# Performance work log

Measured on AMD Instinct MI355X. Metric: run time of the kernel, lower is better.

Reference implementation:

```python
import jax, jax.numpy as jnp
import numpy as np

BATCH, SEQ, D_MODEL = 2, 4096, 1024
D_STATE, EXPAND = 64, 2
D_INNER = D_MODEL * EXPAND


def setup_inputs() -> dict:
    key = jax.random.key(0)
    ks = jax.random.split(key, 12)
    s = 0.02
    return {
        "x": jax.random.normal(ks[0], (BATCH, SEQ, D_MODEL), dtype=jnp.float32),
        "W_in": jax.random.normal(ks[1], (D_MODEL, 2 * D_INNER), dtype=jnp.float32) * s,
        "b_in": jnp.zeros((2 * D_INNER,), dtype=jnp.float32),
        "W_xp": jax.random.normal(ks[2], (D_INNER, D_STATE), dtype=jnp.float32) * s,
        "b_xp": jnp.zeros((D_STATE,), dtype=jnp.float32),
        "W_dt": jax.random.normal(ks[3], (D_INNER, D_MODEL), dtype=jnp.float32) * s,
        "b_dt": jnp.zeros((D_MODEL,), dtype=jnp.float32),
        "W_out": jax.random.normal(ks[4], (D_INNER, D_MODEL), dtype=jnp.float32) * s,
        "b_out": jnp.zeros((D_MODEL,), dtype=jnp.float32),
        "A_log": jax.random.normal(ks[5], (D_STATE,), dtype=jnp.float32),
        "D": jax.random.normal(ks[6], (D_MODEL,), dtype=jnp.float32),
    }


def _silu(v):
    return v * jax.nn.sigmoid(v)


def reference(x, W_in, b_in, W_xp, b_xp, W_dt, b_dt, W_out, b_out, A_log, D):
    # in_proj -> split into inner stream and residual gate
    xr = x @ W_in + b_in                       # [B,S,2*d_inner]
    x_inner, res = jnp.split(xr, 2, axis=-1)   # each [B,S,d_inner]
    x_inner = _silu(x_inner)

    A = -jnp.exp(A_log)                        # [N]
    delta = jax.nn.softplus(x_inner @ W_dt + b_dt)  # [B,S,d_model]
    mean_delta = delta.mean(axis=-1)           # [B,S] (scalar dt per step, as in source)
    a = jnp.exp(A[None, None, :] * mean_delta[..., None])  # [B,S,N] discrete A
    bx = x_inner @ W_xp + b_xp                 # [B,S,N] input injection

    # sequential selective-scan recurrence: state = a_t * state + bx_t
    def step(state, inp):
        a_t, bx_t = inp                        # [B,N] each
        state = a_t * state + bx_t
        return state, state.sum(axis=-1)       # emit per-batch scalar

    init = jnp.zeros((x.shape[0], D_STATE), dtype=x.dtype)
    _, s_sum = jax.lax.scan(step, init, (a.transpose(1, 0, 2), bx.transpose(1, 0, 2)))
    s_sum = s_sum.T                            # [B,S]

    y = s_sum[..., None] * x_inner             # [B,S,d_inner]
    y = y * _silu(res)
    out = y @ W_out + b_out + x * D
    return out
```

## Files before the change

kernel.cpp:

```cpp
#include <hip/hip_runtime.h>

#define SEQ 4096
#define DMODEL 1024
#define DSTATE 64
#define DINNER 2048
#define MROWS 8192
#define NCAT 1152
#define NCHUNK 64
#define LCHUNK 64

typedef __attribute__((ext_vector_type(8))) __bf16 bf16x8;
typedef __attribute__((ext_vector_type(8))) short short8;
typedef __attribute__((ext_vector_type(4))) float floatx4;

__device__ inline float bf2f(short s) {
  union { unsigned u; float f; } c;
  c.u = ((unsigned)(unsigned short)s) << 16;
  return c.f;
}
__device__ inline short f2bf(float f) {
  union { float f; unsigned u; } c; c.f = f;
  unsigned r = 0x7fffu + ((c.u >> 16) & 1u);
  return (short)((c.u + r) >> 16);
}
__device__ inline float silu_f(float v) {
  return v * __builtin_amdgcn_rcpf(1.f + __expf(-v));
}
__device__ inline float softplus_f(float v) {
  return fmaxf(v, 0.f) + log1pf(__expf(-fabsf(v)));
}
__device__ inline void gld_lds16(const void* g, void* l) {
  __builtin_amdgcn_global_load_lds(
      (__attribute__((address_space(1))) void*)g,
      (__attribute__((address_space(3))) void*)l, 16, 0, 0);
}

__device__ inline size_t permOff(int r, int k, int K) {
  return (((size_t)(r >> 4) * (K >> 3) + (k >> 3)) << 7) + ((r & 15) << 3) + (k & 7);
}

#define PP0 4096
#define PP1 (PP0 + 4096)
#define PP2 (PP1 + 2048)
#define PP3 (PP2 + 128)
#define PP4 (PP3 + 2048)

__device__ void tile_transpose_perm(const float* __restrict__ in, short* __restrict__ out,
                                    int R, int C, int bx, int by, float (*tile)[33]) {
  const int tx = threadIdx.x & 31, ty = threadIdx.x >> 5;
  const int cb = bx * 32, rb = by * 32;
#pragma unroll
  for (int i = 0; i < 32; i += 8) {
    int r = rb + ty + i, c = cb + tx;
    tile[ty + i][tx] = (r < R && c < C) ? in[(size_t)r * C + c] : 0.f;
  }
  __syncthreads();
#pragma unroll
  for (int i = 0; i < 32; i += 8) {
    int orow = cb + ty + i, oc = rb + tx;
    if (orow < C && oc < R) out[permOff(orow, oc, R)] = f2bf(tile[tx][ty + i]);
  }
}

__global__ void prepass_kernel(const float* __restrict__ x, short* __restrict__ x_bf,
                               const float* __restrict__ W_in, short* __restrict__ Wt_in,
                               const float* __restrict__ W_dt, const float* __restrict__ W_xp,
                               short* __restrict__ Bcat,
                               const float* __restrict__ W_out, short* __restrict__ Wt_out) {
  __shared__ float tile[32][33];
  const int blk = blockIdx.x;
  if (blk < PP0) {
    int o = blk * 256 + threadIdx.x;
    int m = o & 15, rest = o >> 4;
    int c = rest & 127, p = rest >> 7;
    const float* src = x + ((size_t)(p * 16 + m)) * 1024 + c * 8;
    float4 v0 = ((const float4*)src)[0];
    float4 v1 = ((const float4*)src)[1];
    short8 ov;
    ov[0] = f2bf(v0.x); ov[1] = f2bf(v0.y); ov[2] = f2bf(v0.z); ov[3] = f2bf(v0.w);
    ov[4] = f2bf(v1.x); ov[5] = f2bf(v1.y); ov[6] = f2bf(v1.z); ov[7] = f2bf(v1.w);
    ((short8*)x_bf)[o] = ov;
  } else if (blk < PP1) {
    int t = blk - PP0;
    tile_transpose_perm(W_in, Wt_in, 1024, 4096, t & 127, t >> 7, tile);
  } else if (blk < PP2) {
    int t = blk - PP1;
    tile_transpose_perm(W_dt, Bcat, 2048, 1024, t & 31, t >> 5, tile);
  } else if (blk < PP3) {
    int t = blk - PP2;
    tile_transpose_perm(W_xp, Bcat + (size_t)1024 * DINNER, 2048, 64, t & 1, t >> 1, tile);
  } else {
    int t = blk - PP3;
    tile_transpose_perm(W_out, Wt_out, 2048, 1024, t & 31, t >> 5, tile);
  }
}

template <int MODE, int KTOT, int KSL, int NB, int Z>
__global__ __launch_bounds__(256) void gemm_bt(
    const short* __restrict__ A, const short* __restrict__ Bt,
    const float* __restrict__ bias,
    void* __restrict__ out0, void* __restrict__ out1)
{
  __shared__ __attribute__((aligned(16))) short sA[128 * 64];
  __shared__ __attribute__((aligned(16))) short sB[128 * 64];

  const int tid = threadIdx.x;
  const int lane = tid & 63;
  const int w = tid >> 6;
  const int wr = w >> 1, wc = w & 1;
  const int m = lane & 15, quad = lane >> 4;

  const int xcd = blockIdx.x & 7;
  const int rest = blockIdx.x >> 3;
  constexpr int PXB = 8 * NB;
  const int z = rest / PXB;
  const int q2 = rest - z * PXB;
  const int bM = (xcd * 8 + (q2 & 7)) * 128;
  const int bN = (q2 >> 3) * 128;
  constexpr int N = NB * 128;

  floatx4 acc[4][4] = {};

  const size_t PS = (size_t)KTOT * 16;
  const short* Apan0 = A  + ((size_t)(bM >> 4) + w) * PS + lane * 8;
  const short* Apan1 = Apan0 + 4 * PS;
  const short* Bpan0 = Bt + ((size_t)(bN >> 4) + w) * PS + lane * 8;
  const short* Bpan1 = Bpan0 + 4 * PS;
  short* dA0 = sA + w * 1024;
  short* dA1 = sA + (w + 4) * 1024;
  short* dB0 = sB + w * 1024;
  short* dB1 = sB + (w + 4) * 1024;

  const int kbeg = z * KSL;
  for (int k0 = kbeg; k0 < kbeg + KSL; k0 += 64) {
    __syncthreads();
    const size_t ko = (size_t)k0 * 16;
    gld_lds16(Apan0 + ko,       dA0);
    gld_lds16(Apan0 + ko + 512, dA0 + 512);
    gld_lds16(Apan1 + ko,       dA1);
    gld_lds16(Apan1 + ko + 512, dA1 + 512);
    gld_lds16(Bpan0 + ko,       dB0);
    gld_lds16(Bpan0 + ko + 512, dB0 + 512);
    gld_lds16(Bpan1 + ko,       dB1);
    gld_lds16(Bpan1 + ko + 512, dB1 + 512);
    __syncthreads();
#pragma unroll
    for (int kh = 0; kh < 2; ++kh) {
      bf16x8 af[4], bf[4];
#pragma unroll
      for (int rt = 0; rt < 4; ++rt)
        af[rt] = *(const bf16x8*)(sA + (wr * 4 + rt) * 1024 + (kh * 4 + quad) * 128 + m * 8);
#pragma unroll
      for (int ct = 0; ct < 4; ++ct)
        bf[ct] = *(const bf16x8*)(sB + (wc * 4 + ct) * 1024 + (kh * 4 + quad) * 128 + m * 8);
#pragma unroll
      for (int rt = 0; rt < 4; ++rt)
#pragma unroll
        for (int ct = 0; ct < 4; ++ct)
          acc[rt][ct] = __builtin_amdgcn_mfma_f32_16x16x32_bf16(af[rt], bf[ct], acc[rt][ct], 0, 0, 0);
    }
  }

  const int rowbase = bM + wr * 64;
  const int colbase = bN + wc * 64;

  if (MODE == 0) {
    short* dst = (bN < DINNER) ? (short*)out0 : (short*)out1;
    const int cb = (bN < DINNER) ? colbase : colbase - DINNER;
#pragma unroll
    for (int rt = 0; rt < 4; ++rt) {
      const size_t rowPan = ((size_t)((rowbase >> 4) + rt)) << 8;
#pragma unroll
      for (int ct = 0; ct < 4; ++ct) {
        const int colA = colbase + ct * 16 + m;
        const int colP = cb + ct * 16 + m;
        const size_t base = ((rowPan + (colP >> 3)) << 7) + (colP & 7) + ((size_t)quad * 32);
#pragma unroll
        for (int reg = 0; reg < 4; ++reg) {
          float val = acc[rt][ct][reg] + bias[colA];
          dst[base + reg * 8] = f2bf(silu_f(val));
        }
      }
    }
  } else {
    if (NB == 9 && colbase >= 1088) return;
    short* dst = (short*)out0 + (size_t)z * MROWS * N;
#pragma unroll
    for (int rt = 0; rt < 4; ++rt)
#pragma unroll
      for (int ct = 0; ct < 4; ++ct) {
        const int col = colbase + ct * 16 + m;
#pragma unroll
        for (int reg = 0; reg < 4; ++reg) {
          const int r = rowbase + rt * 16 + quad * 4 + reg;
          dst[(size_t)r * N + col] = f2bf(acc[rt][ct][reg]);
        }
      }
  }
}

template <int MODE, int KTOT, int KSL, int NT, int ZS>
__global__ __launch_bounds__(512, 2) void gemm256(
    const short* __restrict__ A, const short* __restrict__ Bt,
    const float* __restrict__ bias,
    void* __restrict__ out0, void* __restrict__ out1)
{
  __shared__ __attribute__((aligned(16))) short sA[4 * 8192];
  __shared__ __attribute__((aligned(16))) short sB[4 * 8192];

  const int tid = threadIdx.x;
  const int lane = tid & 63;
  const int w = tid >> 6;
  const int wr = w >> 2, wc = w & 3;
  const int m = lane & 15, quad = lane >> 4;

  const int xcd = blockIdx.x & 7;
  const int q = blockIdx.x >> 3;
  const int mt = xcd * 4 + (q & 3);
  const int rest = q >> 2;
  const int ntile = rest % NT;
  const int z = rest / NT;
  const int bM = mt * 256, bN = ntile * 256;
  const int kbeg = z * KSL;

  floatx4 acc[8][4] = {};

  const size_t PS = (size_t)KTOT * 16;
  const short* Ag0 = A  + ((size_t)(bM >> 4) + w) * PS + (size_t)kbeg * 16 + lane * 8;
  const short* Ag1 = Ag0 + 8 * PS;
  const short* Bg0 = Bt + ((size_t)(bN >> 4) + w) * PS + (size_t)kbeg * 16 + lane * 8;
  const short* Bg1 = Bg0 + 8 * PS;

  constexpr int NTILES = KSL / 32;

  auto STAGE_A = [&](int t) {
    const size_t go = (size_t)t << 9;
    short* da = sA + ((t & 3) << 13) + w * 512;
    gld_lds16(Ag0 + go, da);
    gld_lds16(Ag1 + go, da + 4096);
  };
  auto STAGE_B = [&](int t) {
    const size_t go = (size_t)t << 9;
    short* db = sB + ((t & 3) << 13) + w * 512;
    gld_lds16(Bg0 + go, db);
    gld_lds16(Bg1 + go, db + 4096);
  };

  STAGE_A(0); STAGE_B(0); STAGE_A(1); STAGE_B(1); STAGE_A(2); STAGE_B(2);
  asm volatile("s_waitcnt vmcnt(8)" ::: "memory");
  __builtin_amdgcn_s_barrier();

#pragma unroll 1
  for (int t = 0; t < NTILES; ++t) {
    const short* sa = sA + ((t & 3) << 13) + wr * 4096 + quad * 128 + m * 8;
    const short* sb = sB + ((t & 3) << 13) + wc * 2048 + quad * 128 + m * 8;
    bf16x8 af0[4], af1[4], bf[4];

#pragma unroll
    for (int rt = 0; rt < 4; ++rt) af0[rt] = *(const bf16x8*)(sa + rt * 512);
#pragma unroll
    for (int ct = 0; ct < 4; ++ct) bf[ct] = *(const bf16x8*)(sb + ct * 512);
    if (t < NTILES - 3) STAGE_A(t + 3);
    __builtin_amdgcn_sched_barrier(0);
    __builtin_amdgcn_s_barrier();
    __builtin_amdgcn_sched_barrier(0);
    __builtin_amdgcn_s_setprio(1);
#pragma unroll
    for (int rt = 0; rt < 4; ++rt)
#pragma unroll
      for (int ct = 0; ct < 4; ++ct)
        acc[rt][ct] = __builtin_amdgcn_mfma_f32_16x16x32_bf16(af0[rt], bf[ct], acc[rt][ct], 0, 0, 0);
    __builtin_amdgcn_s_setprio(0);
    __builtin_amdgcn_sched_barrier(0);
    __builtin_amdgcn_s_barrier();

#pragma unroll
    for (int rt = 0; rt < 4; ++rt) af1[rt] = *(const bf16x8*)(sa + (4 + rt) * 512);
    if (t < NTILES - 3) STAGE_B(t + 3);
    __builtin_amdgcn_sched_barrier(0);
    __builtin_amdgcn_s_barrier();
    __builtin_amdgcn_sched_barrier(0);
    __builtin_amdgcn_s_setprio(1);
#pragma unroll
    for (int rt = 0; rt < 4; ++rt)
#pragma unroll
      for (int ct = 0; ct < 4; ++ct)
        acc[4 + rt][ct] = __builtin_amdgcn_mfma_f32_16x16x32_bf16(af1[rt], bf[ct], acc[4 + rt][ct], 0, 0, 0);
    __builtin_amdgcn_s_setprio(0);
    __builtin_amdgcn_sched_barrier(0);

    if (t < NTILES - 3)       asm volatile("s_waitcnt vmcnt(8)" ::: "memory");
    else if (t == NTILES - 3) asm volatile("s_waitcnt vmcnt(4)" ::: "memory");
    else if (t == NTILES - 2) asm volatile("s_waitcnt vmcnt(0)" ::: "memory");
    if (t < NTILES - 1) __builtin_amdgcn_s_barrier();
  }

  const int rowbase = bM + wr * 128;
  const int colbase = bN + wc * 64;

  if constexpr (MODE == 0) {
    short* dst = (bN < DINNER) ? (short*)out0 : (short*)out1;
    const int cb = (bN < DINNER) ? colbase : colbase - DINNER;
#pragma unroll
    for (int rt = 0; rt < 8; ++rt) {
      const size_t rowPan = ((size_t)(rowbase >> 4) + rt) << 8;
#pragma unroll
      for (int ct = 0; ct < 4; ++ct) {
        const int colA = colbase + ct * 16 + m;
        const int colP = cb + ct * 16 + m;
        const size_t base = ((rowPan + (colP >> 3)) << 7) + (colP & 7) + ((size_t)quad * 32);
        const float bv = bias[colA];
#pragma unroll
        for (int reg = 0; reg < 4; ++reg) {
          float val = acc[rt][ct][reg] + bv;
          dst[base + reg * 8] = f2bf(silu_f(val));
        }
      }
    }
  } else {
    constexpr int N = NT * 256;
    short* dst = (short*)out0 + (size_t)z * MROWS * N;
#pragma unroll
    for (int rt = 0; rt < 8; ++rt)
#pragma unroll
      for (int ct = 0; ct < 4; ++ct) {
        const int col = colbase + ct * 16 + m;
#pragma unroll
        for (int reg = 0; reg < 4; ++reg) {
          const int r = rowbase + rt * 16 + quad * 4 + reg;
          dst[(size_t)r * N + col] = f2bf(acc[rt][ct][reg]);
        }
      }
  }
}

__global__ void g2_epilogue(const short* __restrict__ p, const float* __restrict__ b_dt,
                            const float* __restrict__ b_xp,
                            float* __restrict__ md_sum, float* __restrict__ bx) {
  const int row = blockIdx.x * 4 + (threadIdx.x >> 6);
  const int lane = threadIdx.x & 63;
  const size_t base0 = (size_t)row * NCAT;
  const size_t base1 = base0 + (size_t)MROWS * NCAT;
  short8 a0 = *(const short8*)(p + base0 + lane * 16);
  short8 a1 = *(const short8*)(p + base0 + lane * 16 + 8);
  short8 c0 = *(const short8*)(p + base1 + lane * 16);
  short8 c1 = *(const short8*)(p + base1 + lane * 16 + 8);
  float s = 0.f;
#pragma unroll
  for (int j = 0; j < 8; ++j) {
    s += softplus_f(bf2f(a0[j]) + bf2f(c0[j]) + b_dt[lane * 16 + j]);
    s += softplus_f(bf2f(a1[j]) + bf2f(c1[j]) + b_dt[lane * 16 + 8 + j]);
  }
  s += __shfl_xor(s, 1);  s += __shfl_xor(s, 2);  s += __shfl_xor(s, 4);
  s += __shfl_xor(s, 8);  s += __shfl_xor(s, 16); s += __shfl_xor(s, 32);
  if (lane == 0) md_sum[row] = s;
  bx[(size_t)row * DSTATE + lane] =
      bf2f(p[base0 + 1024 + lane]) + bf2f(p[base1 + 1024 + lane]) + b_xp[lane];
}

__global__ void g4_epilogue(const short* __restrict__ p, const float* __restrict__ b_out,
                            const float* __restrict__ x, const float* __restrict__ Dv,
                            float* __restrict__ out) {
  const int r = blockIdx.x, c = threadIdx.x * 4;
  const size_t o = (size_t)r * DMODEL + c;
  short4 a0 = *(const short4*)(p + o);
  short4 a1 = *(const short4*)(p + (size_t)MROWS * DMODEL + o);
  float4 xv = *(const float4*)(x + o);
  float4 ov;
  ov.x = bf2f(a0.x) + bf2f(a1.x) + b_out[c + 0] + xv.x * Dv[c + 0];
  ov.y = bf2f(a0.y) + bf2f(a1.y) + b_out[c + 1] + xv.y * Dv[c + 1];
  ov.z = bf2f(a0.z) + bf2f(a1.z) + b_out[c + 2] + xv.z * Dv[c + 2];
  ov.w = bf2f(a0.w) + bf2f(a1.w) + b_out[c + 3] + xv.w * Dv[c + 3];
  *(float4*)(out + o) = ov;
}

__global__ void scan_phase1(const float* __restrict__ md_sum, const float* __restrict__ A_log,
                            const float* __restrict__ bx,
                            float* __restrict__ chunk_prod, float* __restrict__ chunk_end) {
  const int n = threadIdx.x;
  const int c = blockIdx.x & (NCHUNK - 1);
  const int b = blockIdx.x >> 6;
  const float An = -__expf(A_log[n]);
  float prod = 1.f, st = 0.f;
  const int t0 = c * LCHUNK;
#pragma unroll 4
  for (int i = 0; i < LCHUNK; ++i) {
    const int t = t0 + i;
    const float md = md_sum[b * SEQ + t] * (1.f / DMODEL);
    const float a = __expf(An * md);
    st = a * st + bx[((size_t)(b * SEQ + t)) * DSTATE + n];
    prod *= a;
  }
  chunk_prod[(b * NCHUNK + c) * DSTATE + n] = prod;
  chunk_end [(b * NCHUNK + c) * DSTATE + n] = st;
}

__global__ void scan_phase3(const float* __restrict__ md_sum, const float* __restrict__ A_log,
                            const float* __restrict__ bx,
                            const float* __restrict__ chunk_prod,
                            const float* __restrict__ chunk_end,
                            float* __restrict__ s_sum) {
  const int n = threadIdx.x;
  const int c = blockIdx.x & (NCHUNK - 1);
  const int b = blockIdx.x >> 6;
  const float An = -__expf(A_log[n]);
  float st = 0.f;
  for (int cc = 0; cc < c; ++cc) {
    const size_t idx = ((size_t)(b * NCHUNK + cc)) * DSTATE + n;
    st = chunk_prod[idx] * st + chunk_end[idx];
  }
  const int t0 = c * LCHUNK;
#pragma unroll 4
  for (int i = 0; i < LCHUNK; ++i) {
    const int t = t0 + i;
    const float md = md_sum[b * SEQ + t] * (1.f / DMODEL);
    const float a = __expf(An * md);
    st = a * st + bx[((size_t)(b * SEQ + t)) * DSTATE + n];
    float v = st;
    v += __shfl_xor(v, 32); v += __shfl_xor(v, 16); v += __shfl_xor(v, 8);
    v += __shfl_xor(v, 4);  v += __shfl_xor(v, 2);  v += __shfl_xor(v, 1);
    if (n == 0) s_sum[b * SEQ + t] = v;
  }
}

__global__ void ymul_kernel(const short* __restrict__ xi, const short* __restrict__ g,
                            const float* __restrict__ s_sum, short* __restrict__ y) {
  const int o = blockIdx.x * 256 + threadIdx.x;
  const int row = ((o >> 12) << 4) | (o & 15);
  const size_t base = (size_t)o * 8;
  const float s = s_sum[row];
  short8 xv = *(const short8*)(xi + base);
  short8 gv = *(const short8*)(g + base);
  short8 yv;
#pragma unroll
  for (int k = 0; k < 8; ++k) yv[k] = f2bf(s * bf2f(xv[k]) * bf2f(gv[k]));
  *(short8*)(y + base) = yv;
}

extern "C" void kernel_launch(void* const* d_in, const int* in_sizes, int n_in,
                              void* d_out, int out_size, void* d_ws, size_t ws_size,
                              hipStream_t stream) {
  const float* x     = (const float*)d_in[0];
  const float* W_in  = (const float*)d_in[1];
  const float* b_in  = (const float*)d_in[2];
  const float* W_xp  = (const float*)d_in[3];
  const float* b_xp  = (const float*)d_in[4];
  const float* W_dt  = (const float*)d_in[5];
  const float* b_dt  = (const float*)d_in[6];
  const float* W_out = (const float*)d_in[7];
  const float* b_out = (const float*)d_in[8];
  const float* A_log = (const float*)d_in[9];
  const float* Dv    = (const float*)d_in[10];

  char* ws = (char*)d_ws;
  size_t off = 0;
  auto alloc = [&](size_t bytes) -> void* {
    void* p = (void*)(ws + off);
    off += (bytes + 255) & ~(size_t)255;
    return p;
  };
  short* x_bf    = (short*)alloc((size_t)MROWS * DMODEL * 2);
  short* Wt_in   = (short*)alloc((size_t)4096 * 1024 * 2);
  short* Bcat    = (short*)alloc((size_t)NCAT * DINNER * 2);
  short* Wt_out  = (short*)alloc((size_t)1024 * 2048 * 2);
  short* xi      = (short*)alloc((size_t)MROWS * DINNER * 2);
  short* gbuf    = (short*)alloc((size_t)MROWS * DINNER * 2);
  short* ybuf    = (short*)alloc((size_t)MROWS * DINNER * 2);
  short* p2      = (short*)alloc((size_t)2 * MROWS * NCAT * 2);
  float* md_sum  = (float*)alloc((size_t)MROWS * 4);
  float* bx      = (float*)alloc((size_t)MROWS * DSTATE * 4);
  float* cprod   = (float*)alloc((size_t)2 * NCHUNK * DSTATE * 4);
  float* cend    = (float*)alloc((size_t)2 * NCHUNK * DSTATE * 4);
  float* s_sum   = (float*)alloc((size_t)MROWS * 4);

  prepass_kernel<<<PP4, 256, 0, stream>>>(x, x_bf, W_in, Wt_in, W_dt, W_xp, Bcat, W_out, Wt_out);

  gemm256<0, 1024, 1024, 16, 1><<<512, 512, 0, stream>>>(x_bf, Wt_in, b_in, xi, gbuf);
  gemm_bt<1, 2048, 1024, 9, 2><<<1152, 256, 0, stream>>>(xi, Bcat, nullptr, p2, nullptr);
  g2_epilogue<<<MROWS / 4, 256, 0, stream>>>(p2, b_dt, b_xp, md_sum, bx);
  scan_phase1<<<2 * NCHUNK, DSTATE, 0, stream>>>(md_sum, A_log, bx, cprod, cend);
  scan_phase3<<<2 * NCHUNK, DSTATE, 0, stream>>>(md_sum, A_log, bx, cprod, cend, s_sum);
  ymul_kernel<<<MROWS * DINNER / 8 / 256, 256, 0, stream>>>(xi, gbuf, s_sum, ybuf);
  gemm256<1, 2048, 1024, 4, 2><<<256, 512, 0, stream>>>(ybuf, Wt_out, nullptr, xi, nullptr);
  g4_epilogue<<<MROWS, 256, 0, stream>>>(xi, b_out, x, Dv, (float*)d_out);
}
```

Before: 388.5 us.

## Restructure GEMM main loop into double-buffered 64-wide K tiles with quarter-stage prefetch

Replaces the 4-slot, 32-wide K ring buffer for A and B with a single 128KB LDS array holding two 64-wide K tiles, each split into four quarters. Each loop iteration now runs four MFMA phases and prefetches one quarter of the next tile per phase, with explicit s_barrier and lgkmcnt waits. This halves the loop trip count and prefetch depth, aiming to cut per-iteration overhead and barriers per K element. The trade-off is less latency hiding for global loads, one tile ahead instead of three.

```diff
diff --git a/kernel.cpp b/kernel.cpp
--- a/kernel.cpp
+++ b/kernel.cpp
@@ -205,8 +205,7 @@
     const float* __restrict__ bias,
     void* __restrict__ out0, void* __restrict__ out1)
 {
-  __shared__ __attribute__((aligned(16))) short sA[4 * 8192];
-  __shared__ __attribute__((aligned(16))) short sB[4 * 8192];
+  __shared__ __attribute__((aligned(16))) short sLds[65536];
 
   const int tid = threadIdx.x;
   const int lane = tid & 63;
@@ -226,73 +225,114 @@
   floatx4 acc[8][4] = {};
 
   const size_t PS = (size_t)KTOT * 16;
-  const short* Ag0 = A  + ((size_t)(bM >> 4) + w) * PS + (size_t)kbeg * 16 + lane * 8;
-  const short* Ag1 = Ag0 + 8 * PS;
-  const short* Bg0 = Bt + ((size_t)(bN >> 4) + w) * PS + (size_t)kbeg * 16 + lane * 8;
-  const short* Bg1 = Bg0 + 8 * PS;
-
-  constexpr int NTILES = KSL / 32;
-
-  auto STAGE_A = [&](int t) {
-    const size_t go = (size_t)t << 9;
-    short* da = sA + ((t & 3) << 13) + w * 512;
-    gld_lds16(Ag0 + go, da);
-    gld_lds16(Ag1 + go, da + 4096);
+  const short* AgA = A  + ((size_t)(bM >> 4) + w) * PS + (size_t)kbeg * 16 + lane * 8;
+  const short* AgB = AgA + 8 * PS;
+  const short* BgA = Bt + ((size_t)(bN >> 4) + w) * PS + (size_t)kbeg * 16 + lane * 8;
+  const short* BgB = BgA + 8 * PS;
+
+  constexpr int KT = KSL / 64;
+
+  auto STAGE_Q = [&](int t, int qq) {
+    const size_t go = (size_t)t * 1024 + (size_t)(qq >> 1) * 512;
+    short* d = sLds + ((t & 1) << 15) + ((qq & 1) << 14) + ((qq >> 1) << 13) + w * 512;
+    const short* g0 = (qq & 1) ? BgA : AgA;
+    const short* g1 = (qq & 1) ? BgB : AgB;
+    gld_lds16(g0 + go, d);
+    gld_lds16(g1 + go, d + 4096);
   };
-  auto STAGE_B = [&](int t) {
-    const size_t go = (size_t)t << 9;
-    short* db = sB + ((t & 3) << 13) + w * 512;
-    gld_lds16(Bg0 + go, db);
-    gld_lds16(Bg1 + go, db + 4096);
-  };
-
-  STAGE_A(0); STAGE_B(0); STAGE_A(1); STAGE_B(1); STAGE_A(2); STAGE_B(2);
-  asm volatile("s_waitcnt vmcnt(8)" ::: "memory");
-  __builtin_amdgcn_s_barrier();
+
+  const int aoff = wr * 4096 + quad * 128 + m * 8;
+  const int boff = 16384 + wc * 2048 + quad * 128 + m * 8;
+
+  STAGE_Q(0, 0); STAGE_Q(0, 1); STAGE_Q(0, 2); STAGE_Q(0, 3);
+  asm volatile("s_waitcnt vmcnt(4)" ::: "memory");
+  asm volatile("s_barrier" ::: "memory");
 
 #pragma unroll 1
-  for (int t = 0; t < NTILES; ++t) {
-    const short* sa = sA + ((t & 3) << 13) + wr * 4096 + quad * 128 + m * 8;
-    const short* sb = sB + ((t & 3) << 13) + wc * 2048 + quad * 128 + m * 8;
-    bf16x8 af0[4], af1[4], bf[4];
-
-#pragma unroll
-    for (int rt = 0; rt < 4; ++rt) af0[rt] = *(const bf16x8*)(sa + rt * 512);
-#pragma unroll
-    for (int ct = 0; ct < 4; ++ct) bf[ct] = *(const bf16x8*)(sb + ct * 512);
-    if (t < NTILES - 3) STAGE_A(t + 3);
-    __builtin_amdgcn_sched_barrier(0);
-    __builtin_amdgcn_s_barrier();
+  for (int t = 0; t < KT; ++t) {
+    const short* bs = sLds + ((t & 1) << 15);
+    const bool pf = (t + 1 < KT);
+    bf16x8 a[4], b[4];
+
+#pragma unroll
+    for (int rt = 0; rt < 4; ++rt) a[rt] = *(const bf16x8*)(bs + aoff + rt * 512);
+#pragma unroll
+    for (int ct = 0; ct < 4; ++ct) b[ct] = *(const bf16x8*)(bs + boff + ct * 512);
+    if (pf) STAGE_Q(t + 1, 0);
+    __builtin_amdgcn_sched_barrier(0);
+    asm volatile("s_barrier" ::: "memory");
+    asm volatile("s_waitcnt lgkmcnt(0)" ::: "memory");
     __builtin_amdgcn_sched_barrier(0);
     __builtin_amdgcn_s_setprio(1);
 #pragma unroll
     for (int rt = 0; rt < 4; ++rt)
 #pragma unroll
       for (int ct = 0; ct < 4; ++ct)
-        acc[rt][ct] = __builtin_amdgcn_mfma_f32_16x16x32_bf16(af0[rt], bf[ct], acc[rt][ct], 0, 0, 0);
+        acc[rt][ct] = __builtin_amdgcn_mfma_f32_16x16x32_bf16(a[rt], b[ct], acc[rt][ct], 0, 0, 0);
     __builtin_amdgcn_s_setprio(0);
     __builtin_amdgcn_sched_barrier(0);
-    __builtin_amdgcn_s_barrier();
-
-#pragma unroll
-    for (int rt = 0; rt < 4; ++rt) af1[rt] = *(const bf16x8*)(sa + (4 + rt) * 512);
-    if (t < NTILES - 3) STAGE_B(t + 3);
-    __builtin_amdgcn_sched_barrier(0);
-    __builtin_amdgcn_s_barrier();
+    asm volatile("s_barrier" ::: "memory");
+
+#pragma unroll
+    for (int rt = 0; rt < 4; ++rt) a[rt] = *(const bf16x8*)(bs + aoff + (4 + rt) * 512);
+    if (pf) {
+      STAGE_Q(t + 1, 1);
+      asm volatile("s_waitcnt vmcnt(4)" ::: "memory");
+    } else {
+      asm volatile("s_waitcnt vmcnt(0)" ::: "memory");
+    }
+    __builtin_amdgcn_sched_barrier(0);
+    asm volatile("s_barrier" ::: "memory");
+    asm volatile("s_waitcnt lgkmcnt(0)" ::: "memory");
     __builtin_amdgcn_sched_barrier(0);
     __builtin_amdgcn_s_setprio(1);
 #pragma unroll
     for (int rt = 0; rt < 4; ++rt)
 #pragma unroll
       for (int ct = 0; ct < 4; ++ct)
-        acc[4 + rt][ct] = __builtin_amdgcn_mfma_f32_16x16x32_bf16(af1[rt], bf[ct], acc[4 + rt][ct], 0, 0, 0);
+        acc[4 + rt][ct] = __builtin_amdgcn_mfma_f32_16x16x32_bf16(a[rt], b[ct], acc[4 + rt][ct], 0, 0, 0);
     __builtin_amdgcn_s_setprio(0);
     __builtin_amdgcn_sched_barrier(0);
-
-    if (t < NTILES - 3)       asm volatile("s_waitcnt vmcnt(8)" ::: "memory");
-    else if (t == NTILES - 3) asm volatile("s_waitcnt vmcnt(4)" ::: "memory");
-    else if (t == NTILES - 2) asm volatile("s_waitcnt vmcnt(0)" ::: "memory");
-    if (t < NTILES - 1) __builtin_amdgcn_s_barrier();
+    asm volatile("s_barrier" ::: "memory");
+
+#pragma unroll
+    for (int rt = 0; rt < 4; ++rt) a[rt] = *(const bf16x8*)(bs + 8192 + aoff + rt * 512);
+#pragma unroll
+    for (int ct = 0; ct < 4; ++ct) b[ct] = *(const bf16x8*)(bs + 8192 + boff + ct * 512);
+    if (pf) STAGE_Q(t + 1, 2);
+    __builtin_amdgcn_sched_barrier(0);
+    asm volatile("s_barrier" ::: "memory");
+    asm volatile("s_waitcnt lgkmcnt(0)" ::: "memory");
+    __builtin_amdgcn_sched_barrier(0);
+    __builtin_amdgcn_s_setprio(1);
+#pragma unroll
+    for (int rt = 0; rt < 4; ++rt)
+#pragma unroll
+      for (int ct = 0; ct < 4; ++ct)
+        acc[rt][ct] = __builtin_amdgcn_mfma_f32_16x16x32_bf16(a[rt], b[ct], acc[rt][ct], 0, 0, 0);
+    __builtin_amdgcn_s_setprio(0);
+    __builtin_amdgcn_sched_barrier(0);
+    asm volatile("s_barrier" ::: "memory");
+
+#pragma unroll
+    for (int rt = 0; rt < 4; ++rt) a[rt] = *(const bf16x8*)(bs + 8192 + aoff + (4 + rt) * 512);
+    if (pf) {
+      STAGE_Q(t + 1, 3);
+      asm volatile("s_waitcnt vmcnt(4)" ::: "memory");
+    }
+    __builtin_amdgcn_sched_barrier(0);
+    asm volatile("s_barrier" ::: "memory");
+    asm volatile("s_waitcnt lgkmcnt(0)" ::: "memory");
+    __builtin_amdgcn_sched_barrier(0);
+    __builtin_amdgcn_s_setprio(1);
+#pragma unroll
+    for (int rt = 0; rt < 4; ++rt)
+#pragma unroll
+      for (int ct = 0; ct < 4; ++ct)
+        acc[4 + rt][ct] = __builtin_amdgcn_mfma_f32_16x16x32_bf16(a[rt], b[ct], acc[4 + rt][ct], 0, 0, 0);
+    __builtin_amdgcn_s_setprio(0);
+    __builtin_amdgcn_sched_barrier(0);
+    if (pf) asm volatile("s_barrier" ::: "memory");
   }
 
   const int rowbase = bM + wr * 128;
```

Result: no change. 388.6 us (+0.0%).
